# Performance work log

Hardware: AMD Instinct MI355X
Metric: run time of the kernel (lower is better)

Reference implementation:

```python
import jax, jax.numpy as jnp
import numpy as np

K = 3       # kernel size
PAD = 1
STRIDE = 1


def conv2d(x, w, b):
    # Plain dense 3x3 conv, NCHW / OIHW, stride 1, padding 1 (matches nn.Conv2d).
    y = jax.lax.conv_general_dilated(
        x, w, (STRIDE, STRIDE), ((PAD, PAD), (PAD, PAD)),
        dimension_numbers=('NCHW', 'OIHW', 'NCHW'))
    return y + b[None, :, None, None]


def setup_inputs() -> dict:
    key = jax.random.key(0)
    ks = jax.random.split(key, 6)
    B, Cin, Cout, H, W = 8, 256, 256, 48, 48
    x = jax.random.normal(ks[0], (B, Cin, H, W), jnp.float32)
    # main deform-conv weight (kaiming-like scale)
    weight = jax.random.normal(ks[1], (Cout, Cin, K, K), jnp.float32) * (2.0 / (Cin * K * K)) ** 0.5
    # offset/mask convs: torch inits these to zero; we use small random values so the
    # irregular bilinear-gather path is actually exercised.
    off_w = jax.random.normal(ks[2], (2 * K * K, Cin, K, K), jnp.float32) * 0.01
    off_b = jax.random.normal(ks[3], (2 * K * K,), jnp.float32) * 0.1
    mask_w = jax.random.normal(ks[4], (K * K, Cin, K, K), jnp.float32) * 0.01
    mask_b = jnp.zeros((K * K,), jnp.float32)
    return dict(x=x, weight=weight, off_w=off_w, off_b=off_b, mask_w=mask_w, mask_b=mask_b)


def _bilinear_sample(img, py, px):
    # img: [C,H,W]; py,px: [K2,Ho,Wo] fractional sample coords (zero padding outside).
    C, H, W = img.shape
    y0 = jnp.floor(py)
    x0 = jnp.floor(px)
    wy = py - y0
    wx = px - x0

    def gather(yi, xi):
        yc = jnp.clip(yi, 0, H - 1).astype(jnp.int32)
        xc = jnp.clip(xi, 0, W - 1).astype(jnp.int32)
        valid = ((yi >= 0) & (yi <= H - 1) & (xi >= 0) & (xi <= W - 1)).astype(img.dtype)
        return img[:, yc, xc] * valid  # [C,K2,Ho,Wo]

    return (gather(y0, x0) * (1 - wy) * (1 - wx)
            + gather(y0, x0 + 1) * (1 - wy) * wx
            + gather(y0 + 1, x0) * wy * (1 - wx)
            + gather(y0 + 1, x0 + 1) * wy * wx)


def _deform_conv2d(x, offset, mask, weight):
    # Modulated deformable conv v2 (torchvision layout: offset = (dy,dx) pairs per tap).
    B, Cin, H, W = x.shape
    Cout = weight.shape[0]
    Ho, Wo = H, W  # stride 1, pad 1, k 3 -> same spatial size
    ky, kx = jnp.meshgrid(jnp.arange(K), jnp.arange(K), indexing='ij')
    ky = ky.reshape(-1).astype(x.dtype)  # [K2]
    kx = kx.reshape(-1).astype(x.dtype)
    hs = jnp.arange(Ho, dtype=x.dtype) * STRIDE - PAD
    ws = jnp.arange(Wo, dtype=x.dtype) * STRIDE - PAD
    off = offset.reshape(B, K * K, 2, Ho, Wo)
    py = off[:, :, 0] + ky[None, :, None, None] + hs[None, None, :, None]  # [B,K2,Ho,Wo]
    px = off[:, :, 1] + kx[None, :, None, None] + ws[None, None, None, :]
    sampled = jax.vmap(_bilinear_sample)(x, py, px)  # [B,Cin,K2,Ho,Wo]
    vals = sampled * mask[:, None]                   # modulation
    return jnp.einsum('bckhw,ock->bohw', vals, weight.reshape(Cout, Cin, K * K))


def reference(x, weight, off_w, off_b, mask_w, mask_b):
    offset = conv2d(x, off_w, off_b)
    mask = jax.nn.sigmoid(conv2d(x, mask_w, mask_b))
    return _deform_conv2d(x, offset, mask, weight)
```

## Files before the change

### kernel.cpp

```cpp
#include <hip/hip_runtime.h>
#include <cstdint>
#include <cmath>

#define DEV __device__ __forceinline__

typedef float v4f __attribute__((ext_vector_type(4)));
typedef short v8s __attribute__((ext_vector_type(8)));
typedef short v4s __attribute__((ext_vector_type(4)));

static constexpr int HW    = 48 * 48;
static constexpr int NPOS  = 8 * HW;

DEV float bf2f(unsigned short u) {
  unsigned int v = ((unsigned int)u) << 16;
  float f; __builtin_memcpy(&f, &v, 4); return f;
}
DEV unsigned short f2bf(float f) {
  unsigned int u; __builtin_memcpy(&u, &f, 4);
  unsigned int r = (u + 0x7fffu + ((u >> 16) & 1u)) >> 16;
  return (unsigned short)r;
}

DEV void gload16(const void* g, void* l) {
  __builtin_amdgcn_global_load_lds(
      (const __attribute__((address_space(1))) unsigned int*)g,
      (__attribute__((address_space(3))) unsigned int*)l, 16, 0, 0);
}

__global__ __launch_bounds__(256) void k_pre(const float* __restrict__ x,
                                             const float* __restrict__ off_w,
                                             const float* __restrict__ mask_w,
                                             const float* __restrict__ weight,
                                             unsigned short* __restrict__ xT,
                                             unsigned short* __restrict__ Wc2,
                                             unsigned short* __restrict__ zp,
                                             unsigned short* __restrict__ wG) {
  __shared__ float tile[64][65];
  int bid = blockIdx.x, tid = threadIdx.x;
  if (bid < 1152) {
    int ct = bid & 3; int hwt = (bid >> 2) % 36; int b = bid / 144;
    int c0 = ct * 64, hw0 = hwt * 64;
    int tl = tid & 63, tr = tid >> 6;
    const float* xb = x + (size_t)(b * 256 + c0) * 2304 + hw0;
    #pragma unroll
    for (int r = 0; r < 16; r++) {
      int cr = tr + r * 4;
      tile[cr][tl] = xb[(size_t)cr * 2304 + tl];
    }
    __syncthreads();
    unsigned short* xo = xT + ((size_t)b * 2304 + hw0) * 256 + c0;
    #pragma unroll
    for (int r = 0; r < 16; r++) {
      int hr = tr + r * 4;
      xo[(size_t)hr * 256 + tl] = f2bf(tile[tl][hr]);
    }
  } else if (bid < 1440) {
    int i = (bid - 1152) * 256 + tid;
    if (i < 256) zp[i] = 0;
    int o = i / 2304, col = i % 2304;
    int t = col >> 8, c = col & 255;
    float v = 0.f;
    if (o < 18)      v = off_w[(o * 256 + c) * 9 + t];
    else if (o < 27) v = mask_w[((o - 18) * 256 + c) * 9 + t];
    Wc2[i] = f2bf(v);
  } else {
    int co = bid - 1440;
    const float* wsrc = weight + (size_t)co * 2304;
    float* wrow = &tile[0][0];
    for (int k = tid; k < 2304; k += 256) wrow[k] = wsrc[k];
    __syncthreads();
    unsigned short* dst = wG + (size_t)co * 2304;
    #pragma unroll
    for (int k = 0; k < 9; k++)
      dst[k * 256 + tid] = f2bf(wrow[tid * 9 + k]);
  }
}

__global__ __launch_bounds__(256) void k_cg(const unsigned short* __restrict__ Wc2,
                                            const unsigned short* __restrict__ xT,
                                            const unsigned short* __restrict__ zp,
                                            float* __restrict__ parS) {
  __shared__ unsigned short ldsA[32 * 64];
  __shared__ unsigned short ldsB[64 * 64];
  int nt = blockIdx.x, kc = blockIdx.y;
  int n0 = nt * 64;
  int b = n0 / 2304, hw0 = n0 % 2304;
  int tid = threadIdx.x, lane = tid & 63, wid = tid >> 6;
  int r = lane & 15, q = lane >> 4;
  int row0 = tid >> 3;
  int sslot = (tid & 7) ^ (row0 & 7);

  int hwA = hw0 + row0,      hA = hwA / 48, wA = hwA % 48;
  int hwB = hw0 + row0 + 32, hB = hwB / 48, wB = hwB % 48;

  v4f acc0 = (v4f){0.f, 0.f, 0.f, 0.f};
  v4f acc1 = (v4f){0.f, 0.f, 0.f, 0.f};

  #pragma unroll
  for (int tt = 0; tt < 3; tt++) {
    int t = kc * 3 + tt;
    int dy = kc - 1, dx = tt - 1;
    int yA = hA + dy, xA = wA + dx;
    int yB = hB + dy, xB = wB + dx;
    bool vA = ((unsigned)yA < 48u) && ((unsigned)xA < 48u);
    bool vB = ((unsigned)yB < 48u) && ((unsigned)xB < 48u);
    const unsigned short* baseA2 = Wc2 + (size_t)row0 * 2304 + t * 256 + sslot * 8;
    const unsigned short* base0 = vA ? xT + ((size_t)(b * 2304 + yA * 48 + xA) * 256 + sslot * 8)
                                     : zp + sslot * 8;
    const unsigned short* base1 = vB ? xT + ((size_t)(b * 2304 + yB * 48 + xB) * 256 + sslot * 8)
                                     : zp + sslot * 8;
    #pragma unroll
    for (int cq = 0; cq < 4; cq++) {
      int c0s = cq * 64;
      __syncthreads();
      gload16(baseA2 + c0s, ldsA + tid * 8);
      gload16(base0  + c0s, ldsB + tid * 8);
      gload16(base1  + c0s, ldsB + 2048 + tid * 8);
      __syncthreads();
      #pragma unroll
      for (int ki = 0; ki < 2; ki++) {
        int sl = ((ki * 4 + q) ^ (r & 7)) * 8;
        v8s a0 = *(const v8s*)&ldsA[r * 64 + sl];
        v8s a1 = *(const v8s*)&ldsA[(16 + r) * 64 + sl];
        v8s bb = *(const v8s*)&ldsB[(wid * 16 + r) * 64 + sl];
        acc0 = __builtin_amdgcn_mfma_f32_16x16x32_bf16(a0, bb, acc0, 0, 0, 0);
        acc1 = __builtin_amdgcn_mfma_f32_16x16x32_bf16(a1, bb, acc1, 0, 0, 0);
      }
    }
  }

  float* pp = parS + (size_t)kc * 32 * NPOS + n0;
  #pragma unroll
  for (int e = 0; e < 4; e++) {
    pp[(size_t)(q * 4 + e) * NPOS      + wid * 16 + r] = acc0[e];
    pp[(size_t)(16 + q * 4 + e) * NPOS + wid * 16 + r] = acc1[e];
  }
}

__global__ __launch_bounds__(256) void k_fin(const float* __restrict__ parS,
                                             const float* __restrict__ off_b,
                                             const float* __restrict__ mask_b,
                                             float* __restrict__ smp) {
  int k = blockIdx.x / 72;
  int pos = (blockIdx.x % 72) * 256 + threadIdx.x;
  float s0 = 0.f, s1 = 0.f, s2 = 0.f;
  #pragma unroll
  for (int g = 0; g < 3; g++) {
    const float* pg = parS + (size_t)g * 32 * NPOS + pos;
    s0 += pg[(size_t)(2 * k)     * NPOS];
    s1 += pg[(size_t)(2 * k + 1) * NPOS];
    s2 += pg[(size_t)(18 + k)    * NPOS];
  }
  int hw = pos % 2304; int h = hw / 48, w = hw % 48;
  float m = 1.f / (1.f + expf(-(s2 + mask_b[k])));
  float* sp = smp + ((size_t)k * NPOS + pos) * 3;
  sp[0] = s0 + off_b[2 * k]     + (float)(k / 3) + (float)h - 1.f;
  sp[1] = s1 + off_b[2 * k + 1] + (float)(k % 3) + (float)w - 1.f;
  sp[2] = m;
}

__global__ __launch_bounds__(256) void k_gather(const unsigned short* __restrict__ xT,
                                                const float* __restrict__ smp,
                                                unsigned short* __restrict__ val) {
  int raw = blockIdx.x;
  int b = raw & 7;
  int it = raw >> 3;
  int half = threadIdx.x >> 5;
  int lane = threadIdx.x & 31;
  int task = it * 8 + half;
  int k = task % 9, hw = task / 9;
  int pos = b * 2304 + hw;
  const float* sp = smp + ((size_t)k * NPOS + pos) * 3;
  float py = sp[0], px = sp[1], m = sp[2];
  float y0f = floorf(py), x0f = floorf(px);
  float wy = py - y0f, wx = px - x0f;
  int y0 = (int)y0f, x0 = (int)x0f;
  bool vy0 = (y0 >= 0) && (y0 <= 47), vy1 = (y0 >= -1) && (y0 <= 46);
  bool vx0 = (x0 >= 0) && (x0 <= 47), vx1 = (x0 >= -1) && (x0 <= 46);
  int yc0 = min(max(y0, 0), 47), yc1 = min(max(y0 + 1, 0), 47);
  int xc0 = min(max(x0, 0), 47), xc1 = min(max(x0 + 1, 0), 47);
  float w00 = (1.f - wy) * (1.f - wx) * m * (float)(vy0 && vx0);
  float w01 = (1.f - wy) * wx         * m * (float)(vy0 && vx1);
  float w10 = wy         * (1.f - wx) * m * (float)(vy1 && vx0);
  float w11 = wy         * wx         * m * (float)(vy1 && vx1);
  const unsigned short* xb = xT + (size_t)b * 2304 * 256;
  int ch = lane * 8;
  v8s c00 = *(const v8s*)&xb[(yc0 * 48 + xc0) * 256 + ch];
  v8s c01 = *(const v8s*)&xb[(yc0 * 48 + xc1) * 256 + ch];
  v8s c10 = *(const v8s*)&xb[(yc1 * 48 + xc0) * 256 + ch];
  v8s c11 = *(const v8s*)&xb[(yc1 * 48 + xc1) * 256 + ch];
  unsigned short o[8];
  #pragma unroll
  for (int i = 0; i < 8; i++) {
    float v = w00 * bf2f((unsigned short)c00[i]) + w01 * bf2f((unsigned short)c01[i])
            + w10 * bf2f((unsigned short)c10[i]) + w11 * bf2f((unsigned short)c11[i]);
    o[i] = f2bf(v);
  }
  *(v8s*)&val[(size_t)pos * 2304 + k * 256 + ch] = *(const v8s*)o;
}

__global__ __launch_bounds__(256) void k_gemm(const unsigned short* __restrict__ wG,
                                              const unsigned short* __restrict__ val,
                                              float* __restrict__ out) {
  __shared__ unsigned short ldsA[2][128 * 64];
  __shared__ unsigned short ldsB[2][64 * 64];
  int raw = blockIdx.x;
  int xcd = raw & 7, idx = raw >> 3;
  int mt = idx & 1;
  int nt = xcd * 36 + (idx >> 1);
  int co0 = mt * 128, n0 = nt * 64;
  int tid = threadIdx.x, lane = tid & 63, wid = tid >> 6;
  int wm = wid >> 1, wn = wid & 1;
  int r = lane & 15, q = lane >> 4;
  int srow = tid >> 3;
  int sx = ((tid & 7) ^ (srow & 7)) * 8;

  const unsigned short* Ag = wG  + (size_t)(co0 + srow) * 2304 + sx;
  const unsigned short* Bg = val + (size_t)(n0  + srow) * 2304 + sx;

  #define GSTAGE(bufi, k0_) { \
    _Pragma("unroll") for (int i_ = 0; i_ < 4; i_++) \
      gload16(Ag + (k0_) + (size_t)i_ * 32 * 2304, &ldsA[bufi][i_ * 2048 + tid * 8]); \
    _Pragma("unroll") for (int i_ = 0; i_ < 2; i_++) \
      gload16(Bg + (k0_) + (size_t)i_ * 32 * 2304, &ldsB[bufi][i_ * 2048 + tid * 8]); }

  v4f acc[4][2];
  #pragma unroll
  for (int i = 0; i < 4; i++)
    #pragma unroll
    for (int j = 0; j < 2; j++) acc[i][j] = (v4f){0.f, 0.f, 0.f, 0.f};

  GSTAGE(0, 0);
  __syncthreads();

  for (int ks = 0; ks < 36; ks++) {
    int cur = ks & 1;
    if (ks + 1 < 36) GSTAGE(cur ^ 1, (ks + 1) * 64);
    #pragma unroll
    for (int ki = 0; ki < 2; ki++) {
      int sl = ((ki * 4 + q) ^ (r & 7)) * 8;
      v8s af[4], bf[2];
      #pragma unroll
      for (int fm = 0; fm < 4; fm++)
        af[fm] = *(const v8s*)&ldsA[cur][(wm * 64 + fm * 16 + r) * 64 + sl];
      #pragma unroll
      for (int fn = 0; fn < 2; fn++)
        bf[fn] = *(const v8s*)&ldsB[cur][(wn * 32 + fn * 16 + r) * 64 + sl];
      #pragma unroll
      for (int fm = 0; fm < 4; fm++)
        #pragma unroll
        for (int fn = 0; fn < 2; fn++)
          acc[fm][fn] = __builtin_amdgcn_mfma_f32_16x16x32_bf16(af[fm], bf[fn], acc[fm][fn], 0, 0, 0);
    }
    __syncthreads();
  }

  int bimg = n0 / 2304, hw0 = n0 % 2304;
  float* op = out + (size_t)bimg * (256 * 2304) + hw0;
  #pragma unroll
  for (int fm = 0; fm < 4; fm++) {
    int co = co0 + wm * 64 + fm * 16 + q * 4;
    #pragma unroll
    for (int fn = 0; fn < 2; fn++) {
      int nn = wn * 32 + fn * 16 + r;
      #pragma unroll
      for (int e = 0; e < 4; e++)
        op[(size_t)(co + e) * 2304 + nn] = acc[fm][fn][e];
    }
  }
  #undef GSTAGE
}

extern "C" void kernel_launch(void* const* d_in, const int* in_sizes, int n_in,
                              void* d_out, int out_size, void* d_ws, size_t ws_size,
                              hipStream_t stream) {
  const float* x      = (const float*)d_in[0];
  const float* weight = (const float*)d_in[1];
  const float* off_w  = (const float*)d_in[2];
  const float* off_b  = (const float*)d_in[3];
  const float* mask_w = (const float*)d_in[4];
  const float* mask_b = (const float*)d_in[5];
  float* out = (float*)d_out;
  char* ws = (char*)d_ws;

  unsigned short* xT   = (unsigned short*)(ws);
  unsigned short* wG   = (unsigned short*)(ws + 9437184);
  unsigned short* Wc2  = (unsigned short*)(ws + 10616832);
  unsigned short* zp   = (unsigned short*)(ws + 10764288);
  float*          smp  = (float*)(ws + 10764800);
  float*          parS = (float*)(ws + 12755456);
  unsigned short* val  = (unsigned short*)(ws + 12755456);

  hipLaunchKernelGGL(k_pre,    dim3(1696),     dim3(256), 0, stream,
                     x, off_w, mask_w, weight, xT, Wc2, zp, wG);
  hipLaunchKernelGGL(k_cg,     dim3(288, 3),   dim3(256), 0, stream, Wc2, xT, zp, parS);
  hipLaunchKernelGGL(k_fin,    dim3(648),      dim3(256), 0, stream, parS, off_b, mask_b, smp);
  hipLaunchKernelGGL(k_gather, dim3(20736),    dim3(256), 0, stream, xT, smp, val);
  hipLaunchKernelGGL(k_gemm,   dim3(576),      dim3(256), 0, stream, wG, val, out);
}
```

Baseline: 83.84 us.

## Double-buffer offset-conv LDS loads and fold finalize into gather kernel

The offset/mask conv kernel now double-buffers its LDS tiles, prefetching the next chunk while MFMAs run on the current one. This halves the barriers per stage and overlaps global-to-LDS loads with compute. The separate finalize kernel is removed; the gather kernel now sums the three partial sums, applies bias and sigmoid, and builds the sample coordinates itself. That saves one launch and the intermediate smp write and read, but each gather thread does redundant parS reads that 32 lanes share and recomputes expf.

```diff
diff --git a/kernel.cpp b/kernel.cpp
--- a/kernel.cpp
+++ b/kernel.cpp
@@ -80,8 +80,8 @@
                                             const unsigned short* __restrict__ xT,
                                             const unsigned short* __restrict__ zp,
                                             float* __restrict__ parS) {
-  __shared__ unsigned short ldsA[32 * 64];
-  __shared__ unsigned short ldsB[64 * 64];
+  __shared__ unsigned short ldsA[2][32 * 64];
+  __shared__ unsigned short ldsB[2][64 * 64];
   int nt = blockIdx.x, kc = blockIdx.y;
   int n0 = nt * 64;
   int b = n0 / 2304, hw0 = n0 % 2304;
@@ -93,9 +93,9 @@
   int hwA = hw0 + row0,      hA = hwA / 48, wA = hwA % 48;
   int hwB = hw0 + row0 + 32, hB = hwB / 48, wB = hwB % 48;
 
-  v4f acc0 = (v4f){0.f, 0.f, 0.f, 0.f};
-  v4f acc1 = (v4f){0.f, 0.f, 0.f, 0.f};
-
+  const unsigned short* bA[3];
+  const unsigned short* b0[3];
+  const unsigned short* b1[3];
   #pragma unroll
   for (int tt = 0; tt < 3; tt++) {
     int t = kc * 3 + tt;
@@ -104,29 +104,38 @@
     int yB = hB + dy, xB = wB + dx;
     bool vA = ((unsigned)yA < 48u) && ((unsigned)xA < 48u);
     bool vB = ((unsigned)yB < 48u) && ((unsigned)xB < 48u);
-    const unsigned short* baseA2 = Wc2 + (size_t)row0 * 2304 + t * 256 + sslot * 8;
-    const unsigned short* base0 = vA ? xT + ((size_t)(b * 2304 + yA * 48 + xA) * 256 + sslot * 8)
-                                     : zp + sslot * 8;
-    const unsigned short* base1 = vB ? xT + ((size_t)(b * 2304 + yB * 48 + xB) * 256 + sslot * 8)
-                                     : zp + sslot * 8;
-    #pragma unroll
-    for (int cq = 0; cq < 4; cq++) {
-      int c0s = cq * 64;
-      __syncthreads();
-      gload16(baseA2 + c0s, ldsA + tid * 8);
-      gload16(base0  + c0s, ldsB + tid * 8);
-      gload16(base1  + c0s, ldsB + 2048 + tid * 8);
-      __syncthreads();
-      #pragma unroll
-      for (int ki = 0; ki < 2; ki++) {
-        int sl = ((ki * 4 + q) ^ (r & 7)) * 8;
-        v8s a0 = *(const v8s*)&ldsA[r * 64 + sl];
-        v8s a1 = *(const v8s*)&ldsA[(16 + r) * 64 + sl];
-        v8s bb = *(const v8s*)&ldsB[(wid * 16 + r) * 64 + sl];
-        acc0 = __builtin_amdgcn_mfma_f32_16x16x32_bf16(a0, bb, acc0, 0, 0, 0);
-        acc1 = __builtin_amdgcn_mfma_f32_16x16x32_bf16(a1, bb, acc1, 0, 0, 0);
-      }
-    }
+    bA[tt] = Wc2 + (size_t)row0 * 2304 + t * 256 + sslot * 8;
+    b0[tt] = vA ? xT + ((size_t)(b * 2304 + yA * 48 + xA) * 256 + sslot * 8)
+                : zp + sslot * 8;
+    b1[tt] = vB ? xT + ((size_t)(b * 2304 + yB * 48 + xB) * 256 + sslot * 8)
+                : zp + sslot * 8;
+  }
+
+  #define CSTAGE(bufi, s_) { \
+    gload16(bA[(s_) >> 2] + ((s_) & 3) * 64, &ldsA[bufi][tid * 8]); \
+    gload16(b0[(s_) >> 2] + ((s_) & 3) * 64, &ldsB[bufi][tid * 8]); \
+    gload16(b1[(s_) >> 2] + ((s_) & 3) * 64, &ldsB[bufi][2048 + tid * 8]); }
+
+  v4f acc0 = (v4f){0.f, 0.f, 0.f, 0.f};
+  v4f acc1 = (v4f){0.f, 0.f, 0.f, 0.f};
+
+  CSTAGE(0, 0);
+  __syncthreads();
+
+  #pragma unroll
+  for (int s = 0; s < 12; s++) {
+    int cur = s & 1;
+    if (s + 1 < 12) CSTAGE(cur ^ 1, s + 1);
+    #pragma unroll
+    for (int ki = 0; ki < 2; ki++) {
+      int sl = ((ki * 4 + q) ^ (r & 7)) * 8;
+      v8s a0 = *(const v8s*)&ldsA[cur][r * 64 + sl];
+      v8s a1 = *(const v8s*)&ldsA[cur][(16 + r) * 64 + sl];
+      v8s bb = *(const v8s*)&ldsB[cur][(wid * 16 + r) * 64 + sl];
+      acc0 = __builtin_amdgcn_mfma_f32_16x16x32_bf16(a0, bb, acc0, 0, 0, 0);
+      acc1 = __builtin_amdgcn_mfma_f32_16x16x32_bf16(a1, bb, acc1, 0, 0, 0);
+    }
+    __syncthreads();
   }
 
   float* pp = parS + (size_t)kc * 32 * NPOS + n0;
@@ -135,32 +144,13 @@
     pp[(size_t)(q * 4 + e) * NPOS      + wid * 16 + r] = acc0[e];
     pp[(size_t)(16 + q * 4 + e) * NPOS + wid * 16 + r] = acc1[e];
   }
-}
-
-__global__ __launch_bounds__(256) void k_fin(const float* __restrict__ parS,
-                                             const float* __restrict__ off_b,
-                                             const float* __restrict__ mask_b,
-                                             float* __restrict__ smp) {
-  int k = blockIdx.x / 72;
-  int pos = (blockIdx.x % 72) * 256 + threadIdx.x;
-  float s0 = 0.f, s1 = 0.f, s2 = 0.f;
-  #pragma unroll
-  for (int g = 0; g < 3; g++) {
-    const float* pg = parS + (size_t)g * 32 * NPOS + pos;
-    s0 += pg[(size_t)(2 * k)     * NPOS];
-    s1 += pg[(size_t)(2 * k + 1) * NPOS];
-    s2 += pg[(size_t)(18 + k)    * NPOS];
-  }
-  int hw = pos % 2304; int h = hw / 48, w = hw % 48;
-  float m = 1.f / (1.f + expf(-(s2 + mask_b[k])));
-  float* sp = smp + ((size_t)k * NPOS + pos) * 3;
-  sp[0] = s0 + off_b[2 * k]     + (float)(k / 3) + (float)h - 1.f;
-  sp[1] = s1 + off_b[2 * k + 1] + (float)(k % 3) + (float)w - 1.f;
-  sp[2] = m;
+  #undef CSTAGE
 }
 
 __global__ __launch_bounds__(256) void k_gather(const unsigned short* __restrict__ xT,
-                                                const float* __restrict__ smp,
+                                                const float* __restrict__ parS,
+                                                const float* __restrict__ off_b,
+                                                const float* __restrict__ mask_b,
                                                 unsigned short* __restrict__ val) {
   int raw = blockIdx.x;
   int b = raw & 7;
@@ -170,8 +160,20 @@
   int task = it * 8 + half;
   int k = task % 9, hw = task / 9;
   int pos = b * 2304 + hw;
-  const float* sp = smp + ((size_t)k * NPOS + pos) * 3;
-  float py = sp[0], px = sp[1], m = sp[2];
+
+  float s0 = 0.f, s1 = 0.f, s2 = 0.f;
+  #pragma unroll
+  for (int g = 0; g < 3; g++) {
+    const float* pg = parS + (size_t)g * 32 * NPOS + pos;
+    s0 += pg[(size_t)(2 * k)     * NPOS];
+    s1 += pg[(size_t)(2 * k + 1) * NPOS];
+    s2 += pg[(size_t)(18 + k)    * NPOS];
+  }
+  int h = hw / 48, w = hw % 48;
+  float m  = 1.f / (1.f + expf(-(s2 + mask_b[k])));
+  float py = s0 + off_b[2 * k]     + (float)(k / 3) + (float)h - 1.f;
+  float px = s1 + off_b[2 * k + 1] + (float)(k % 3) + (float)w - 1.f;
+
   float y0f = floorf(py), x0f = floorf(px);
   float wy = py - y0f, wx = px - x0f;
   int y0 = (int)y0f, x0 = (int)x0f;
@@ -287,14 +289,12 @@
   unsigned short* wG   = (unsigned short*)(ws + 9437184);
   unsigned short* Wc2  = (unsigned short*)(ws + 10616832);
   unsigned short* zp   = (unsigned short*)(ws + 10764288);
-  float*          smp  = (float*)(ws + 10764800);
-  float*          parS = (float*)(ws + 12755456);
-  unsigned short* val  = (unsigned short*)(ws + 12755456);
+  float*          parS = (float*)(ws + 10764800);
+  unsigned short* val  = (unsigned short*)(ws + 17842688);
 
   hipLaunchKernelGGL(k_pre,    dim3(1696),     dim3(256), 0, stream,
                      x, off_w, mask_w, weight, xT, Wc2, zp, wG);
   hipLaunchKernelGGL(k_cg,     dim3(288, 3),   dim3(256), 0, stream, Wc2, xT, zp, parS);
-  hipLaunchKernelGGL(k_fin,    dim3(648),      dim3(256), 0, stream, parS, off_b, mask_b, smp);
-  hipLaunchKernelGGL(k_gather, dim3(20736),    dim3(256), 0, stream, xT, smp, val);
+  hipLaunchKernelGGL(k_gather, dim3(20736),    dim3(256), 0, stream, xT, parS, off_b, mask_b, val);
   hipLaunchKernelGGL(k_gemm,   dim3(576),      dim3(256), 0, stream, wG, val, out);
 }
```

Result: slower. 88.30 us (+5.3%).
